# Optimization experiments

Measured on AMD Instinct MI355X. Metric: run time of the kernel, lower is better.

The kernel has to match this reference:

```python
import jax, jax.numpy as jnp
import numpy as np

T, BLOCK, SIG = 4096, 1024, 1024
LAM = 0.25


def _lstm_cell(x, h, c, Wih, Whh, bih, bhh):
    # PyTorch LSTM gate order: i, f, g, o
    gates = x @ Wih.T + h @ Whh.T + bih + bhh  # [1, 4H]
    i, f, g, o = jnp.split(gates, 4, axis=-1)
    i = jax.nn.sigmoid(i)
    f = jax.nn.sigmoid(f)
    g = jnp.tanh(g)
    o = jax.nn.sigmoid(o)
    c_new = f * c + i * g
    h_new = o * jnp.tanh(c_new)
    return h_new, c_new


def setup_inputs() -> dict:
    key = jax.random.key(0)
    ks = jax.random.split(key, 9)
    ke = 1.0 / np.sqrt(SIG)
    kd = 1.0 / np.sqrt(BLOCK)
    inputs = jax.random.normal(ks[0], (T, 1, BLOCK), dtype=jnp.float32)
    enc_Wih = jax.random.uniform(ks[1], (4 * SIG, BLOCK), jnp.float32, -ke, ke)
    enc_Whh = jax.random.uniform(ks[2], (4 * SIG, SIG), jnp.float32, -ke, ke)
    enc_bih = jax.random.uniform(ks[3], (4 * SIG,), jnp.float32, -ke, ke)
    enc_bhh = jax.random.uniform(ks[4], (4 * SIG,), jnp.float32, -ke, ke)
    dec_Wih = jax.random.uniform(ks[5], (4 * BLOCK, SIG), jnp.float32, -kd, kd)
    dec_Whh = jax.random.uniform(ks[6], (4 * BLOCK, BLOCK), jnp.float32, -kd, kd)
    dec_bih = jax.random.uniform(ks[7], (4 * BLOCK,), jnp.float32, -kd, kd)
    dec_bhh = jax.random.uniform(ks[8], (4 * BLOCK,), jnp.float32, -kd, kd)
    return {"inputs": inputs, "enc_Wih": enc_Wih, "enc_Whh": enc_Whh,
            "enc_bih": enc_bih, "enc_bhh": enc_bhh, "dec_Wih": dec_Wih,
            "dec_Whh": dec_Whh, "dec_bih": dec_bih, "dec_bhh": dec_bhh}


def reference(inputs, enc_Wih, enc_Whh, enc_bih, enc_bhh,
              dec_Wih, dec_Whh, dec_bih, dec_bhh):
    H = enc_Whh.shape[1]
    B = inputs.shape[-1]

    # encode: full-sequence LSTM, zero initial state, batch=1
    def enc_step(carry, x):
        h, c = carry
        h, c = _lstm_cell(x, h, c, enc_Wih, enc_Whh, enc_bih, enc_bhh)
        return (h, c), h

    h0 = jnp.zeros((1, H), inputs.dtype)
    c0 = jnp.zeros((1, H), inputs.dtype)
    _, signal = jax.lax.scan(enc_step, (h0, c0), inputs)  # [T, 1, H]

    # decode: one LSTM step per i; h0 reset to inputs[i], cell state carried
    def dec_step(c, xs):
        x, h_init = xs  # x = signal[i+1], h_init = inputs[i]
        h, c = _lstm_cell(x, h_init, c, dec_Wih, dec_Whh, dec_bih, dec_bhh)
        return c, h

    cdec0 = jnp.zeros((1, B), inputs.dtype)
    _, decoded = jax.lax.scan(dec_step, cdec0, (signal[1:], inputs[:-1]))  # [T-1, 1, B]

    target = inputs[1:]
    mse_loss = jnp.mean((decoded - target) ** 2)
    l1_reg = jnp.sum(jnp.abs(signal)) / signal.size
    loss = mse_loss + LAM * l1_reg
    return loss, mse_loss, l1_reg
```

## Files before the change

### kernel.cpp

```cpp
#include <hip/hip_runtime.h>
#include <math.h>

#define TSTEPS 4096
#define DIM 1024
#define GDIM 4096
#define ENC_NB 64
#define NSEG 64
#define SEGLEN 64

typedef short bf16x8 __attribute__((ext_vector_type(8)));
typedef float f32x4 __attribute__((ext_vector_type(4)));
typedef unsigned int uint4v __attribute__((ext_vector_type(4)));

__device__ __forceinline__ float sigmoidf_(float x) {
    return 1.0f / (1.0f + expf(-x));
}

__device__ __forceinline__ void loadcvt(const float* __restrict__ p,
                                        bf16x8& hi, bf16x8& lo)
{
    float4 a = *(const float4*)p;
    float4 b = *(const float4*)(p + 4);
    float f[8] = {a.x, a.y, a.z, a.w, b.x, b.y, b.z, b.w};
    uint4v hw, lw;
    #pragma unroll
    for (int j = 0; j < 4; ++j) {
        unsigned u0 = __float_as_uint(f[2*j]);
        unsigned u1 = __float_as_uint(f[2*j+1]);
        unsigned m0 = u0 & 0xffff0000u;
        unsigned m1 = u1 & 0xffff0000u;
        float r0 = f[2*j]   - __uint_as_float(m0);
        float r1 = f[2*j+1] - __uint_as_float(m1);
        hw[j] = __builtin_amdgcn_perm(u1, u0, 0x07060302u);
        lw[j] = __builtin_amdgcn_perm(__float_as_uint(r1), __float_as_uint(r0),
                                      0x07060302u);
    }
    hi = __builtin_bit_cast(bf16x8, hw);
    lo = __builtin_bit_cast(bf16x8, lw);
}

template<bool DUAL>
__global__ __launch_bounds__(256)
void gemm_split(const float* __restrict__ A1, const float* __restrict__ B1,
                const float* __restrict__ A2, const float* __restrict__ B2,
                const float* __restrict__ bias1, const float* __restrict__ bias2,
                float* __restrict__ C, int N)
{
    const int lane = threadIdx.x & 63;
    const int wid  = threadIdx.x >> 6;
    const int m0 = blockIdx.y * 128 + (wid >> 1) * 64;
    const int n0 = blockIdx.x * 128 + (wid & 1) * 64;
    const int rA   = m0 + (lane & 15);
    const int cB   = n0 + (lane & 15);
    const int koff = (lane >> 4) * 8;

    f32x4 acc[4][4] = {};

    const int npass = DUAL ? 2 : 1;
    for (int pass = 0; pass < npass; ++pass) {
        const float* __restrict__ A = (DUAL && pass) ? A2 : A1;
        const float* __restrict__ B = (DUAL && pass) ? B2 : B1;
        for (int k0 = 0; k0 < 1024; k0 += 32) {
            bf16x8 ah[4], al[4], bh[4], bl[4];
            #pragma unroll
            for (int i = 0; i < 4; ++i)
                loadcvt(A + (size_t)(rA + i * 16) * 1024 + k0 + koff, ah[i], al[i]);
            #pragma unroll
            for (int j = 0; j < 4; ++j)
                loadcvt(B + (size_t)(cB + j * 16) * 1024 + k0 + koff, bh[j], bl[j]);
            #pragma unroll
            for (int i = 0; i < 4; ++i)
                #pragma unroll
                for (int j = 0; j < 4; ++j) {
                    acc[i][j] = __builtin_amdgcn_mfma_f32_16x16x32_bf16(
                        ah[i], bh[j], acc[i][j], 0, 0, 0);
                    acc[i][j] = __builtin_amdgcn_mfma_f32_16x16x32_bf16(
                        ah[i], bl[j], acc[i][j], 0, 0, 0);
                    acc[i][j] = __builtin_amdgcn_mfma_f32_16x16x32_bf16(
                        al[i], bh[j], acc[i][j], 0, 0, 0);
                }
        }
    }

    const int er = (lane >> 4) * 4;
    const int ec = lane & 15;
    #pragma unroll
    for (int j = 0; j < 4; ++j) {
        int col = n0 + j * 16 + ec;
        float bb = bias1[col] + bias2[col];
        #pragma unroll
        for (int i = 0; i < 4; ++i) {
            int rowb = m0 + i * 16 + er;
            #pragma unroll
            for (int r = 0; r < 4; ++r)
                C[(size_t)(rowb + r) * N + col] = acc[i][j][r] + bb;
        }
    }
}

__global__ __launch_bounds__(1024)
void encoder_scan(const float* __restrict__ Xg,
                  const float* __restrict__ Whh,
                  float* __restrict__ signal,
                  unsigned long long* __restrict__ slots,
                  float* __restrict__ l1_acc)
{
    const int b = blockIdx.x;
    const int t = threadIdx.x;
    const int hbase = b * 16;
    const int w = t >> 6;
    const int j = t & 63;
    const int q = j >> 4;
    const int sub = j & 15;
    const int ch = hbase + w;
    const int grow = q * 1024 + ch;

    float4 wreg[16];
    {
        const float4* wrow = (const float4*)(Whh + (size_t)grow * 1024 + sub * 64);
        #pragma unroll
        for (int i = 0; i < 16; ++i) wreg[i] = wrow[i];
    }

    __shared__ float hls[2][16 * 68];
    __shared__ float hstage[16];

    float c = 0.f;
    float l1 = 0.f;

    for (int step = 0; step < TSTEPS; ++step) {
        const unsigned us = (unsigned)step;
        float xg = 0.f;
        if (sub == 0) xg = Xg[(size_t)step * GDIM + grow];

        const unsigned long long* sp = slots + (size_t)(step & 1) * 1024 + t;
        unsigned long long v;
        while (true) {
            v = __hip_atomic_load(sp, __ATOMIC_RELAXED, __HIP_MEMORY_SCOPE_AGENT);
            if ((unsigned)(v >> 32) >= us) break;
            __builtin_amdgcn_s_sleep(1);
        }

        float* hb = hls[step & 1];
        hb[w * 68 + j] = __uint_as_float((unsigned)v);
        __syncthreads();

        float s = 0.f;
        const float* hv = hb + sub * 68;
        #pragma unroll
        for (int i = 0; i < 16; ++i) {
            float4 h4 = *(const float4*)(hv + i * 4);
            s = fmaf(wreg[i].x, h4.x, s); s = fmaf(wreg[i].y, h4.y, s);
            s = fmaf(wreg[i].z, h4.z, s); s = fmaf(wreg[i].w, h4.w, s);
        }
        s += __shfl_xor(s, 1);
        s += __shfl_xor(s, 2);
        s += __shfl_xor(s, 4);
        s += __shfl_xor(s, 8);

        float act = 0.f;
        if (sub == 0) {
            float pre = s + xg;
            act = (q == 2) ? tanhf(pre) : sigmoidf_(pre);
        }
        float fv = __shfl(act, 16);
        float gv = __shfl(act, 32);
        float ov = __shfl(act, 48);
        if (j == 0) {
            c = fmaf(fv, c, act * gv);
            hstage[w] = ov * tanhf(c);
        }
        __syncthreads();

        if (t < 16) {
            float h = hstage[t];
            unsigned long long pv =
                ((unsigned long long)(us + 1) << 32) | __float_as_uint(h);
            __hip_atomic_store(slots + (size_t)((step + 1) & 1) * 1024 + hbase + t,
                               pv, __ATOMIC_RELAXED, __HIP_MEMORY_SCOPE_AGENT);
            signal[(size_t)step * DIM + hbase + t] = h;
            l1 += fabsf(h);
        }
    }
    if (t < 16) {
        #pragma unroll
        for (int off = 8; off >= 1; off >>= 1) l1 += __shfl_xor(l1, off);
        if (t == 0) atomicAdd(l1_acc, l1);
    }
}

__global__ __launch_bounds__(256)
void dec_compose(const float* __restrict__ G, float* __restrict__ Aseg,
                 float* __restrict__ Bseg)
{
    const int j = blockIdx.x * 256 + threadIdx.x;
    const int s = blockIdx.y;
    const int t0 = s * SEGLEN;
    const int t1 = min(t0 + SEGLEN, TSTEPS - 1);
    float A = 1.f, Bv = 0.f;
    for (int t = t0; t < t1; ++t) {
        const float* g = G + (size_t)t * GDIM;
        float iv = sigmoidf_(g[j]);
        float fv = sigmoidf_(g[j + 1024]);
        float gv = tanhf(g[j + 2048]);
        A *= fv;
        Bv = fmaf(fv, Bv, iv * gv);
    }
    Aseg[s * DIM + j] = A;
    Bseg[s * DIM + j] = Bv;
}

__global__ __launch_bounds__(1024)
void dec_scan(const float* __restrict__ Aseg, const float* __restrict__ Bseg,
              float* __restrict__ cinit)
{
    const int j = threadIdx.x;
    float c = 0.f;
    for (int s = 0; s < NSEG; ++s) {
        cinit[s * DIM + j] = c;
        c = fmaf(Aseg[s * DIM + j], c, Bseg[s * DIM + j]);
    }
}

__global__ __launch_bounds__(256)
void dec_emit(const float* __restrict__ G, const float* __restrict__ inp,
              const float* __restrict__ cinit, float* __restrict__ mse_acc)
{
    const int j = blockIdx.x * 256 + threadIdx.x;
    const int s = blockIdx.y;
    const int t0 = s * SEGLEN;
    const int t1 = min(t0 + SEGLEN, TSTEPS - 1);
    float c = cinit[s * DIM + j];
    float acc = 0.f;
    for (int t = t0; t < t1; ++t) {
        const float* g = G + (size_t)t * GDIM;
        float iv = sigmoidf_(g[j]);
        float fv = sigmoidf_(g[j + 1024]);
        float gv = tanhf(g[j + 2048]);
        float ov = sigmoidf_(g[j + 3072]);
        c = fmaf(fv, c, iv * gv);
        float d = ov * tanhf(c);
        float diff = d - inp[(size_t)(t + 1) * DIM + j];
        acc = fmaf(diff, diff, acc);
    }
    #pragma unroll
    for (int off = 32; off >= 1; off >>= 1) acc += __shfl_xor(acc, off);
    if ((threadIdx.x & 63) == 0) atomicAdd(mse_acc, acc);
}

__global__ void finalize(const float* __restrict__ scal, float* __restrict__ out)
{
    float mse = scal[0] / ((float)(TSTEPS - 1) * (float)DIM);
    float l1  = scal[1] / ((float)TSTEPS * (float)DIM);
    out[0] = mse + 0.25f * l1;
    out[1] = mse;
    out[2] = l1;
}

extern "C" void kernel_launch(void* const* d_in, const int* in_sizes, int n_in,
                              void* d_out, int out_size, void* d_ws, size_t ws_size,
                              hipStream_t stream)
{
    const float* inputs  = (const float*)d_in[0];
    const float* enc_Wih = (const float*)d_in[1];
    const float* enc_Whh = (const float*)d_in[2];
    const float* enc_bih = (const float*)d_in[3];
    const float* enc_bhh = (const float*)d_in[4];
    const float* dec_Wih = (const float*)d_in[5];
    const float* dec_Whh = (const float*)d_in[6];
    const float* dec_bih = (const float*)d_in[7];
    const float* dec_bhh = (const float*)d_in[8];
    float* out = (float*)d_out;

    float* ws = (float*)d_ws;
    float* gates  = ws;
    float* signal = ws + (size_t)16777216;
    unsigned long long* slots =
        (unsigned long long*)(ws + (size_t)20972544);
    float* scal   = ws + (size_t)20976640;
    float* Aseg   = ws + (size_t)20976648;
    float* Bseg   = ws + (size_t)21042184;
    float* cinit  = ws + (size_t)21107720;
    float* mse_acc = scal + 0;
    float* l1_acc  = scal + 1;

    hipMemsetAsync(ws + (size_t)20971520, 0, (size_t)(1024 + 4096 + 8) * 4, stream);

    dim3 b256(256);
    gemm_split<false><<<dim3(32, 32), b256, 0, stream>>>(
        inputs, enc_Wih, nullptr, nullptr, enc_bih, enc_bhh, gates, GDIM);
    encoder_scan<<<dim3(ENC_NB), dim3(1024), 0, stream>>>(
        gates, enc_Whh, signal, slots, l1_acc);
    gemm_split<true><<<dim3(32, 32), b256, 0, stream>>>(
        signal + DIM, dec_Wih, inputs, dec_Whh, dec_bih, dec_bhh, gates, GDIM);
    dec_compose<<<dim3(4, NSEG), b256, 0, stream>>>(gates, Aseg, Bseg);
    dec_scan<<<dim3(1), dim3(1024), 0, stream>>>(Aseg, Bseg, cinit);
    dec_emit<<<dim3(4, NSEG), b256, 0, stream>>>(gates, inputs, cinit, mse_acc);
    finalize<<<dim3(1), dim3(1), 0, stream>>>(scal, out);
}
```

Measured before the change: 8.975 ms.

## Compute all four LSTM gates per thread in a 256-thread encoder scan

The encoder recurrence drops from 1024 to 256 threads per block, with each thread keeping four gate-row slices of Whh in registers. That is 256 floats, which relies on launch_bounds(256,1) allowing a large VGPR budget. Each thread polls four h slots and writes them to shared memory as one float4. The four gate pre-activations are computed with independent FMA chains, which removes the cross-lane shuffles of gate activations and the double-buffered shared h. The aim is to shorten the serial per-step latency through cheaper barriers and fewer waves, at the cost of heavy register pressure and possible spills.

Measured after the change: 14.70 ms. +63.8%, slower.

```diff
diff --git a/kernel.cpp b/kernel.cpp
--- a/kernel.cpp
+++ b/kernel.cpp
@@ -98,7 +98,7 @@
     }
 }
 
-__global__ __launch_bounds__(1024)
+__global__ __launch_bounds__(256, 1)
 void encoder_scan(const float* __restrict__ Xg,
                   const float* __restrict__ Whh,
                   float* __restrict__ signal,
@@ -108,21 +108,20 @@
     const int b = blockIdx.x;
     const int t = threadIdx.x;
     const int hbase = b * 16;
-    const int w = t >> 6;
-    const int j = t & 63;
-    const int q = j >> 4;
-    const int sub = j & 15;
-    const int ch = hbase + w;
-    const int grow = q * 1024 + ch;
-
-    float4 wreg[16];
-    {
-        const float4* wrow = (const float4*)(Whh + (size_t)grow * 1024 + sub * 64);
-        #pragma unroll
-        for (int i = 0; i < 16; ++i) wreg[i] = wrow[i];
-    }
-
-    __shared__ float hls[2][16 * 68];
+    const int hi = t >> 4;
+    const int sub = t & 15;
+    const int ch = hbase + hi;
+
+    float4 wreg[4][16];
+    #pragma unroll
+    for (int q = 0; q < 4; ++q) {
+        const float4* wrow =
+            (const float4*)(Whh + (size_t)(q * 1024 + ch) * 1024 + sub * 64);
+        #pragma unroll
+        for (int i = 0; i < 16; ++i) wreg[q][i] = wrow[i];
+    }
+
+    __shared__ float hls[16 * 68];
     __shared__ float hstage[16];
 
     float c = 0.f;
@@ -130,45 +129,59 @@
 
     for (int step = 0; step < TSTEPS; ++step) {
         const unsigned us = (unsigned)step;
-        float xg = 0.f;
-        if (sub == 0) xg = Xg[(size_t)step * GDIM + grow];
-
-        const unsigned long long* sp = slots + (size_t)(step & 1) * 1024 + t;
-        unsigned long long v;
+
+        float xg0 = 0.f, xg1 = 0.f, xg2 = 0.f, xg3 = 0.f;
+        if (sub == 0) {
+            const float* xr = Xg + (size_t)step * GDIM + ch;
+            xg0 = xr[0]; xg1 = xr[1024]; xg2 = xr[2048]; xg3 = xr[3072];
+        }
+
+        const unsigned long long* sp = slots + (size_t)(step & 1) * 1024 + 4 * t;
+        unsigned long long v0, v1, v2, v3;
         while (true) {
-            v = __hip_atomic_load(sp, __ATOMIC_RELAXED, __HIP_MEMORY_SCOPE_AGENT);
-            if ((unsigned)(v >> 32) >= us) break;
+            v0 = __hip_atomic_load(sp + 0, __ATOMIC_RELAXED, __HIP_MEMORY_SCOPE_AGENT);
+            v1 = __hip_atomic_load(sp + 1, __ATOMIC_RELAXED, __HIP_MEMORY_SCOPE_AGENT);
+            v2 = __hip_atomic_load(sp + 2, __ATOMIC_RELAXED, __HIP_MEMORY_SCOPE_AGENT);
+            v3 = __hip_atomic_load(sp + 3, __ATOMIC_RELAXED, __HIP_MEMORY_SCOPE_AGENT);
+            unsigned tmin = min(min((unsigned)(v0 >> 32), (unsigned)(v1 >> 32)),
+                                min((unsigned)(v2 >> 32), (unsigned)(v3 >> 32)));
+            if (tmin >= us) break;
             __builtin_amdgcn_s_sleep(1);
         }
-
-        float* hb = hls[step & 1];
-        hb[w * 68 + j] = __uint_as_float((unsigned)v);
+        *(float4*)(hls + hi * 68 + 4 * sub) =
+            make_float4(__uint_as_float((unsigned)v0), __uint_as_float((unsigned)v1),
+                        __uint_as_float((unsigned)v2), __uint_as_float((unsigned)v3));
         __syncthreads();
 
-        float s = 0.f;
-        const float* hv = hb + sub * 68;
+        float a0 = 0.f, a1 = 0.f, a2 = 0.f, a3 = 0.f;
+        const float* hv = hls + sub * 68;
         #pragma unroll
         for (int i = 0; i < 16; ++i) {
             float4 h4 = *(const float4*)(hv + i * 4);
-            s = fmaf(wreg[i].x, h4.x, s); s = fmaf(wreg[i].y, h4.y, s);
-            s = fmaf(wreg[i].z, h4.z, s); s = fmaf(wreg[i].w, h4.w, s);
-        }
-        s += __shfl_xor(s, 1);
-        s += __shfl_xor(s, 2);
-        s += __shfl_xor(s, 4);
-        s += __shfl_xor(s, 8);
-
-        float act = 0.f;
+            a0 = fmaf(wreg[0][i].x, h4.x, a0); a0 = fmaf(wreg[0][i].y, h4.y, a0);
+            a0 = fmaf(wreg[0][i].z, h4.z, a0); a0 = fmaf(wreg[0][i].w, h4.w, a0);
+            a1 = fmaf(wreg[1][i].x, h4.x, a1); a1 = fmaf(wreg[1][i].y, h4.y, a1);
+            a1 = fmaf(wreg[1][i].z, h4.z, a1); a1 = fmaf(wreg[1][i].w, h4.w, a1);
+            a2 = fmaf(wreg[2][i].x, h4.x, a2); a2 = fmaf(wreg[2][i].y, h4.y, a2);
+            a2 = fmaf(wreg[2][i].z, h4.z, a2); a2 = fmaf(wreg[2][i].w, h4.w, a2);
+            a3 = fmaf(wreg[3][i].x, h4.x, a3); a3 = fmaf(wreg[3][i].y, h4.y, a3);
+            a3 = fmaf(wreg[3][i].z, h4.z, a3); a3 = fmaf(wreg[3][i].w, h4.w, a3);
+        }
+        #pragma unroll
+        for (int m = 1; m <= 8; m <<= 1) {
+            a0 += __shfl_xor(a0, m);
+            a1 += __shfl_xor(a1, m);
+            a2 += __shfl_xor(a2, m);
+            a3 += __shfl_xor(a3, m);
+        }
+
         if (sub == 0) {
-            float pre = s + xg;
-            act = (q == 2) ? tanhf(pre) : sigmoidf_(pre);
-        }
-        float fv = __shfl(act, 16);
-        float gv = __shfl(act, 32);
-        float ov = __shfl(act, 48);
-        if (j == 0) {
-            c = fmaf(fv, c, act * gv);
-            hstage[w] = ov * tanhf(c);
+            float iv = sigmoidf_(a0 + xg0);
+            float fv = sigmoidf_(a1 + xg1);
+            float gv = tanhf(a2 + xg2);
+            float ov = sigmoidf_(a3 + xg3);
+            c = fmaf(fv, c, iv * gv);
+            hstage[hi] = ov * tanhf(c);
         }
         __syncthreads();
 
@@ -289,7 +302,7 @@
     dim3 b256(256);
     gemm_split<false><<<dim3(32, 32), b256, 0, stream>>>(
         inputs, enc_Wih, nullptr, nullptr, enc_bih, enc_bhh, gates, GDIM);
-    encoder_scan<<<dim3(ENC_NB), dim3(1024), 0, stream>>>(
+    encoder_scan<<<dim3(ENC_NB), b256, 0, stream>>>(
         gates, enc_Whh, signal, slots, l1_acc);
     gemm_split<true><<<dim3(32, 32), b256, 0, stream>>>(
         signal + DIM, dec_Wih, inputs, dec_Whh, dec_bih, dec_bhh, gates, GDIM);
```
